# Kernel optimization log

Hardware: AMD Instinct MI355X
Metric: run time of the kernel (lower is better)

Reference implementation:

```python
import jax, jax.numpy as jnp
import numpy as np

B, S = 512, 512
VOCAB, E, H1, H2, NTAGS = 50000, 20, 30, 50, 45


def _xavier_scale(fan_in, fan_out):
    return float(np.sqrt(2.0 / (fan_in + fan_out)))


def setup_inputs() -> dict:
    key = jax.random.key(0)
    ks = jax.random.split(key, 32)
    n = lambda i, shape, s=1.0: jax.random.normal(ks[i], shape, dtype=jnp.float32) * s
    w = 0.1  # weight scale
    emb_f1 = n(0, (VOCAB, E), w).at[0].set(0.0)  # padding_idx=0
    emb_b1 = n(1, (VOCAB, E), w).at[0].set(0.0)
    xs1 = _xavier_scale(B, H1)
    xs2 = _xavier_scale(B, H2)
    inp = {
        "x": jax.random.randint(ks[2], (B, S), 0, VOCAB, dtype=jnp.int64),
        "emb_f1": emb_f1, "emb_b1": emb_b1,
        "h0_f1": n(3, (B, H1), xs1), "c0_f1": n(4, (B, H1), xs1),
        "Wih_f1": n(5, (4 * H1, E), w), "Whh_f1": n(6, (4 * H1, H1), w),
        "bih_f1": n(7, (4 * H1,), w), "bhh_f1": n(8, (4 * H1,), w),
        "h0_b1": n(9, (B, H1), xs1), "c0_b1": n(10, (B, H1), xs1),
        "Wih_b1": n(11, (4 * H1, E), w), "Whh_b1": n(12, (4 * H1, H1), w),
        "bih_b1": n(13, (4 * H1,), w), "bhh_b1": n(14, (4 * H1,), w),
        "h0_f2": n(15, (B, H2), xs2), "c0_f2": n(16, (B, H2), xs2),
        "Wih_f2": n(17, (4 * H2, 2 * H1), w), "Whh_f2": n(18, (4 * H2, H2), w),
        "bih_f2": n(19, (4 * H2,), w), "bhh_f2": n(20, (4 * H2,), w),
        "h0_b2": n(21, (B, H2), xs2), "c0_b2": n(22, (B, H2), xs2),
        "Wih_b2": n(23, (4 * H2, 2 * H1), w), "Whh_b2": n(24, (4 * H2, H2), w),
        "bih_b2": n(25, (4 * H2,), w), "bhh_b2": n(26, (4 * H2,), w),
        "lin_w": n(27, (NTAGS, 2 * H2), w), "lin_b": n(28, (NTAGS,), w),
    }
    return inp


def _run_lstm(seq, h0, c0, Wih, Whh, bih, bhh, forward):
    """PyTorch LSTMCell recurrence over seq (B,S,D). Replicates the original's
    quirks: backward dir appends hidden states in reversed time order, and the
    (S,B,H) stack is .view()-ed into (B,S,H) without transposing."""
    b, s, _ = seq.shape
    h = h0.shape[-1]
    xs = jnp.swapaxes(seq, 0, 1)  # (S,B,D)

    def step(carry, xt):
        hh, cc = carry
        g = xt @ Wih.T + bih + hh @ Whh.T + bhh  # (B, 4H), gate order i,f,g,o
        i, f, gg, o = jnp.split(g, 4, axis=-1)
        cc = jax.nn.sigmoid(f) * cc + jax.nn.sigmoid(i) * jnp.tanh(gg)
        hh = jax.nn.sigmoid(o) * jnp.tanh(cc)
        return (hh, cc), hh

    _, hs = jax.lax.scan(step, (h0, c0), xs, reverse=not forward)  # hs[i] ~ time i
    if not forward:
        hs = hs[::-1]  # torch appended in processing (reversed-time) order
    return hs.reshape(b, s, h)  # faithful buggy view (S,B,H) -> (B,S,H)


def reference(x, emb_f1, emb_b1,
              h0_f1, c0_f1, Wih_f1, Whh_f1, bih_f1, bhh_f1,
              h0_b1, c0_b1, Wih_b1, Whh_b1, bih_b1, bhh_b1,
              h0_f2, c0_f2, Wih_f2, Whh_f2, bih_f2, bhh_f2,
              h0_b2, c0_b2, Wih_b2, Whh_b2, bih_b2, bhh_b2,
              lin_w, lin_b):
    f1 = _run_lstm(emb_f1[x], h0_f1, c0_f1, Wih_f1, Whh_f1, bih_f1, bhh_f1, True)
    b1 = _run_lstm(emb_b1[x], h0_b1, c0_b1, Wih_b1, Whh_b1, bih_b1, bhh_b1, False)
    l1 = jnp.concatenate([f1, b1], axis=2)  # (B,S,2*H1)
    f2 = _run_lstm(l1, h0_f2, c0_f2, Wih_f2, Whh_f2, bih_f2, bhh_f2, True)
    b2 = _run_lstm(l1, h0_b2, c0_b2, Wih_b2, Whh_b2, bih_b2, bhh_b2, False)
    l2 = jnp.concatenate([f2, b2], axis=2)  # (B,S,2*H2)
    return l2 @ lin_w.T + lin_b  # (B,S,NTAGS)
```

## Files before the change

kernel.cpp:

```cpp
#include <hip/hip_runtime.h>
#include <hip/hip_bf16.h>

typedef __hip_bfloat16 bf16;
typedef __attribute__((ext_vector_type(8))) short short8;
typedef __attribute__((ext_vector_type(4))) float float4v;
typedef unsigned short ushort_t;

#define BB 512
#define SS 512
#define EE 20
#define H1C 30
#define H2C 50
#define NTC 45

#define BAR() asm volatile("s_waitcnt lgkmcnt(0)\n\ts_barrier" ::: "memory")

#if __has_builtin(__builtin_amdgcn_exp2f)
#define EXP2(x) __builtin_amdgcn_exp2f(x)
#else
#define EXP2(x) exp2f(x)
#endif
#if __has_builtin(__builtin_amdgcn_rcpf)
#define RCPF(x) __builtin_amdgcn_rcpf(x)
#else
#define RCPF(x) (1.0f / (x))
#endif

__device__ __forceinline__ float sigf(float v) {
    return RCPF(1.0f + EXP2(-1.4426950408889634f * v));
}
__device__ __forceinline__ float tanh_(float v) {
    return 2.0f * RCPF(1.0f + EXP2(-2.8853900817779268f * v)) - 1.0f;
}

__device__ __forceinline__ ushort_t f2bf(float f) {
    unsigned u = __float_as_uint(f);
    unsigned r = u + 0x7FFFu + ((u >> 16) & 1u);
    return (ushort_t)(r >> 16);
}
__device__ __forceinline__ float bf2f(ushort_t s) { return __uint_as_float(((unsigned)s) << 16); }

__device__ __forceinline__ float ldG(const void* p, int i, int f32) {
    if (f32) return ((const float*)p)[i];
    return bf2f(((const ushort_t*)p)[i]);
}
__device__ __forceinline__ int ldTok(const void* x, int i, int x64) {
    const int* xi = (const int*)x;
    return x64 ? xi[2 * i] : xi[i];
}

__global__ void detect_kernel(const void* bih, const void* x, int* flags) {
    if (threadIdx.x == 0 && blockIdx.x == 0) {
        const ushort_t* u = (const ushort_t*)bih;
        int isf = 0;
        for (int i = 0; i < 120; i++) {
            float v = fabsf(bf2f(u[i]));
            if (!(v < 16.0f)) isf = 1;
        }
        flags[0] = isf;
        const int* xi = (const int*)x;
        int orv = 0;
        for (int i = 1; i < 32; i += 2) orv |= xi[i];
        flags[1] = (orv == 0) ? 1 : 0;
    }
}

struct XV4 { float v[4]; };

__global__ __launch_bounds__(128) void lstm1_kernel(
    const void* __restrict__ x,
    const void* __restrict__ emb_f, const void* __restrict__ emb_b,
    const void* __restrict__ h0_f, const void* __restrict__ c0_f,
    const void* __restrict__ Wih_f, const void* __restrict__ Whh_f,
    const void* __restrict__ bih_f, const void* __restrict__ bhh_f,
    const void* __restrict__ h0_b, const void* __restrict__ c0_b,
    const void* __restrict__ Wih_b, const void* __restrict__ Whh_b,
    const void* __restrict__ bih_b, const void* __restrict__ bhh_b,
    ushort_t* __restrict__ hsf, ushort_t* __restrict__ hsb,
    const int* __restrict__ flags)
{
    const int f32v = flags[0], x64 = flags[1];
    const int wg = blockIdx.x, dir = wg >> 5, j0 = (wg & 31) << 4, tid = threadIdx.x;
    const int wave = tid >> 6, lane = tid & 63, li = lane & 15, quad = lane >> 4;

    const void* emb = dir ? emb_b : emb_f;
    const void* h0  = dir ? h0_b  : h0_f;
    const void* c0  = dir ? c0_b  : c0_f;
    const void* Wih = dir ? Wih_b : Wih_f;
    const void* Whh = dir ? Whh_b : Whh_f;
    const void* bih = dir ? bih_b : bih_f;
    const void* bhh = dir ? bhh_b : bhh_f;
    ushort_t* hs = dir ? hsb : hsf;

    __shared__ __align__(16) ushort_t Af[2][2][64][8];
    __shared__ int toks[16][SS];

    for (int idx = tid; idx < 16 * SS; idx += 128) {
        int r = idx >> 9, t = idx & (SS - 1);
        toks[r][t] = ldTok(x, (j0 + r) * SS + t, x64);
    }
    for (int idx = tid; idx < 2 * 2 * 64 * 8; idx += 128) ((ushort_t*)Af)[idx] = 0;

    const int n = wave * 16 + li;
    const bool nok = n < H1C;

    short8 bhi[4][2], blo[4][2];
    float bias_g[4];
    #pragma unroll
    for (int g = 0; g < 4; g++) {
        const int wrow = g * H1C + n;
        bias_g[g] = nok ? (ldG(bih, wrow, f32v) + ldG(bhh, wrow, f32v)) : 0.f;
        #pragma unroll
        for (int kt = 0; kt < 2; kt++) {
            short8 hi, lo;
            #pragma unroll
            for (int j = 0; j < 8; j++) {
                int k = kt * 32 + quad * 8 + j;
                float w = 0.f;
                if (nok) {
                    if (k < EE) w = ldG(Wih, wrow * EE + k, f32v);
                    else if (k < EE + H1C) w = ldG(Whh, wrow * H1C + (k - EE), f32v);
                }
                ushort_t h = f2bf(w);
                hi[j] = (short)h;
                lo[j] = (short)f2bf(w - bf2f(h));
            }
            bhi[g][kt] = hi; blo[g][kt] = lo;
        }
    }

    const int kh = EE + n;
    const int khk = kh >> 5, khg = (kh & 31) >> 3, khj = kh & 7;
    const int lrow = tid / 5, lc = tid - lrow * 5, k0 = lc * 4;
    const bool ldr = tid < 80;
    const int t0 = dir ? SS - 1 : 0, dt = dir ? -1 : 1;

    __syncthreads();

    float creg[4];
    #pragma unroll
    for (int r = 0; r < 4; r++) {
        const int m = quad * 4 + r;
        creg[r] = nok ? ldG(c0, (j0 + m) * H1C + n, f32v) : 0.f;
        ushort_t hb = nok ? f2bf(ldG(h0, (j0 + m) * H1C + n, f32v)) : 0;
        Af[0][khk][khg * 16 + m][khj] = hb;
    }
    XV4 xA, xB;
    if (ldr) {
        int tok = toks[lrow][t0];
        #pragma unroll
        for (int jj = 0; jj < 4; jj++)
            Af[0][0][(k0 >> 3) * 16 + lrow][(k0 & 7) + jj] = f2bf(ldG(emb, tok * EE + k0 + jj, f32v));
        int tok1 = toks[lrow][t0 + dt];
        #pragma unroll
        for (int jj = 0; jj < 4; jj++) xA.v[jj] = ldG(emb, tok1 * EE + k0 + jj, f32v);
    }
    __syncthreads();

    auto step = [&](int it, XV4& xin, XV4& xout) {
        const int t = t0 + dt * it;
        const int cur = it & 1, nxt = cur ^ 1;
        BAR();
        short8 af0 = *(const short8*)&Af[cur][0][lane][0];
        short8 af1 = *(const short8*)&Af[cur][1][lane][0];
        if (ldr && it + 2 < SS) {
            int tok = toks[lrow][t + 2 * dt];
            #pragma unroll
            for (int jj = 0; jj < 4; jj++) xout.v[jj] = ldG(emb, tok * EE + k0 + jj, f32v);
        }
        float4v acc[4];
        #pragma unroll
        for (int g = 0; g < 4; g++) {
            float4v a; a[0] = a[1] = a[2] = a[3] = bias_g[g];
            a = __builtin_amdgcn_mfma_f32_16x16x32_bf16(af0, bhi[g][0], a, 0, 0, 0);
            a = __builtin_amdgcn_mfma_f32_16x16x32_bf16(af0, blo[g][0], a, 0, 0, 0);
            a = __builtin_amdgcn_mfma_f32_16x16x32_bf16(af1, bhi[g][1], a, 0, 0, 0);
            a = __builtin_amdgcn_mfma_f32_16x16x32_bf16(af1, blo[g][1], a, 0, 0, 0);
            acc[g] = a;
        }
        ushort_t hb[4];
        #pragma unroll
        for (int r = 0; r < 4; r++) {
            float gi = acc[0][r], gf = acc[1][r], gg = acc[2][r], go = acc[3][r];
            float c = sigf(gf) * creg[r] + sigf(gi) * tanh_(gg);
            float h = sigf(go) * tanh_(c);
            creg[r] = c;
            hb[r] = nok ? f2bf(h) : 0;
            hs[((size_t)(j0 + quad * 4 + r) * SS + t) * 32 + n] = hb[r];
        }
        if (it + 1 < SS) {
            #pragma unroll
            for (int r = 0; r < 4; r++) Af[nxt][khk][khg * 16 + quad * 4 + r][khj] = hb[r];
            if (ldr) {
                #pragma unroll
                for (int jj = 0; jj < 4; jj++)
                    Af[nxt][0][(k0 >> 3) * 16 + lrow][(k0 & 7) + jj] = f2bf(xin.v[jj]);
            }
        }
    };
    for (int it = 0; it < SS; it += 2) { step(it, xA, xB); step(it + 1, xB, xA); }
}

__global__ __launch_bounds__(256) void lstm2_kernel(
    const ushort_t* __restrict__ hs1f, const ushort_t* __restrict__ hs1b,
    const void* __restrict__ h0_f, const void* __restrict__ c0_f,
    const void* __restrict__ Wih_f, const void* __restrict__ Whh_f,
    const void* __restrict__ bih_f, const void* __restrict__ bhh_f,
    const void* __restrict__ h0_b, const void* __restrict__ c0_b,
    const void* __restrict__ Wih_b, const void* __restrict__ Whh_b,
    const void* __restrict__ bih_b, const void* __restrict__ bhh_b,
    ushort_t* __restrict__ hsf, ushort_t* __restrict__ hsb,
    const int* __restrict__ flags)
{
    const int f32v = flags[0];
    const int wg = blockIdx.x, dir = wg >> 5, cb = (wg & 31) << 4, tid = threadIdx.x;
    const int wave = tid >> 6, lane = tid & 63, li = lane & 15, quad = lane >> 4;

    const void* h0  = dir ? h0_b  : h0_f;
    const void* c0  = dir ? c0_b  : c0_f;
    const void* Wih = dir ? Wih_b : Wih_f;
    const void* Whh = dir ? Whh_b : Whh_f;
    const void* bih = dir ? bih_b : bih_f;
    const void* bhh = dir ? bhh_b : bhh_f;
    ushort_t* hs = dir ? hsb : hsf;

    __shared__ __align__(16) ushort_t Af[2][4][64][8];
    for (int idx = tid; idx < 2 * 4 * 64 * 8; idx += 256) ((ushort_t*)Af)[idx] = 0;

    const int n = wave * 16 + li;
    const bool nok = n < H2C;

    short8 bhi[4][4], blo[4][4];
    float bias_g[4];
    #pragma unroll
    for (int g = 0; g < 4; g++) {
        const int wrow = g * H2C + n;
        bias_g[g] = nok ? (ldG(bih, wrow, f32v) + ldG(bhh, wrow, f32v)) : 0.f;
        #pragma unroll
        for (int kt = 0; kt < 4; kt++) {
            short8 hi, lo;
            #pragma unroll
            for (int j = 0; j < 8; j++) {
                int k = kt * 32 + quad * 8 + j;
                float w = 0.f;
                if (nok) {
                    if (k < H1C) w = ldG(Wih, wrow * (2 * H1C) + k, f32v);
                    else if (k >= 32 && k < 32 + H1C) w = ldG(Wih, wrow * (2 * H1C) + H1C + (k - 32), f32v);
                    else if (k >= 64 && k < 64 + H2C) w = ldG(Whh, wrow * H2C + (k - 64), f32v);
                }
                ushort_t h = f2bf(w);
                hi[j] = (short)h;
                lo[j] = (short)f2bf(w - bf2f(h));
            }
            bhi[g][kt] = hi; blo[g][kt] = lo;
        }
    }

    const int kh = 64 + n;
    const int khk = kh >> 5, khg = (kh & 31) >> 3, khj = kh & 7;
    const int lrow = tid >> 4, k0 = (tid & 15) * 4;
    const int t0 = dir ? SS - 1 : 0, dt = dir ? -1 : 1;

    auto loadX = [&](int c) -> ushort4 {
        const int a = cb + lrow;
        if (k0 < 32)
            return *(const ushort4*)&hs1f[((size_t)c * SS + a) * 32 + k0];
        else
            return *(const ushort4*)&hs1b[((size_t)c * SS + (SS - 1 - a)) * 32 + (k0 - 32)];
    };

    __syncthreads();

    float creg[4];
    #pragma unroll
    for (int r = 0; r < 4; r++) {
        const int m = quad * 4 + r;
        creg[r] = nok ? ldG(c0, (cb + m) * H2C + n, f32v) : 0.f;
        ushort_t hb = nok ? f2bf(ldG(h0, (cb + m) * H2C + n, f32v)) : 0;
        Af[0][khk][khg * 16 + m][khj] = hb;
    }
    {
        ushort4 xi = loadX(t0);
        const int kg = (k0 & 31) >> 3, kt = k0 >> 5, jb = k0 & 7;
        Af[0][kt][kg * 16 + lrow][jb + 0] = xi.x;
        Af[0][kt][kg * 16 + lrow][jb + 1] = xi.y;
        Af[0][kt][kg * 16 + lrow][jb + 2] = xi.z;
        Af[0][kt][kg * 16 + lrow][jb + 3] = xi.w;
    }
    ushort4 xA = loadX(t0 + dt), xB;
    __syncthreads();

    auto step = [&](int it, ushort4& xin, ushort4& xout) {
        const int c = t0 + dt * it;
        const int cur = it & 1, nxt = cur ^ 1;
        BAR();
        short8 af[4];
        #pragma unroll
        for (int kt = 0; kt < 4; kt++) af[kt] = *(const short8*)&Af[cur][kt][lane][0];
        if (it + 2 < SS) xout = loadX(c + 2 * dt);
        float4v acc[4];
        #pragma unroll
        for (int g = 0; g < 4; g++) {
            float4v a; a[0] = a[1] = a[2] = a[3] = bias_g[g];
            #pragma unroll
            for (int kt = 0; kt < 4; kt++) {
                a = __builtin_amdgcn_mfma_f32_16x16x32_bf16(af[kt], bhi[g][kt], a, 0, 0, 0);
                a = __builtin_amdgcn_mfma_f32_16x16x32_bf16(af[kt], blo[g][kt], a, 0, 0, 0);
            }
            acc[g] = a;
        }
        ushort_t hb[4];
        #pragma unroll
        for (int r = 0; r < 4; r++) {
            float gi = acc[0][r], gf = acc[1][r], gg = acc[2][r], go = acc[3][r];
            float cc = sigf(gf) * creg[r] + sigf(gi) * tanh_(gg);
            float h = sigf(go) * tanh_(cc);
            creg[r] = cc;
            hb[r] = nok ? f2bf(h) : 0;
        }
        ushort4 h4; h4.x = hb[0]; h4.y = hb[1]; h4.z = hb[2]; h4.w = hb[3];
        *(ushort4*)&hs[((size_t)c * 64 + n) * SS + cb + quad * 4] = h4;
        if (it + 1 < SS) {
            #pragma unroll
            for (int r = 0; r < 4; r++) Af[nxt][khk][khg * 16 + quad * 4 + r][khj] = hb[r];
            const int kg = (k0 & 31) >> 3, kt = k0 >> 5, jb = k0 & 7;
            Af[nxt][kt][kg * 16 + lrow][jb + 0] = xin.x;
            Af[nxt][kt][kg * 16 + lrow][jb + 1] = xin.y;
            Af[nxt][kt][kg * 16 + lrow][jb + 2] = xin.z;
            Af[nxt][kt][kg * 16 + lrow][jb + 3] = xin.w;
        }
    };
    for (int it = 0; it < SS; it += 2) { step(it, xA, xB); step(it + 1, xB, xA); }
}

__global__ __launch_bounds__(256) void lin_kernel(
    const ushort_t* __restrict__ hs2f, const ushort_t* __restrict__ hs2b,
    const void* __restrict__ lw, const void* __restrict__ lb,
    void* __restrict__ out, const int* __restrict__ flags)
{
    const int f32v = flags[0];
    const int tid = threadIdx.x, wave = tid >> 6, lane = tid & 63, li = lane & 15, quad = lane >> 4;

    __shared__ __align__(16) ushort_t Af[4][4][64][8];
    for (int idx = tid; idx < 4 * 4 * 64 * 8; idx += 256) ((ushort_t*)Af)[idx] = 0;

    short8 bhi[3][4], blo[3][4];
    float biasv[3];
    #pragma unroll
    for (int nt = 0; nt < 3; nt++) {
        const int nn = nt * 16 + li;
        const bool nok = nn < NTC;
        biasv[nt] = nok ? ldG(lb, nn, f32v) : 0.f;
        #pragma unroll
        for (int kt = 0; kt < 4; kt++) {
            short8 hi, lo;
            #pragma unroll
            for (int j = 0; j < 8; j++) {
                int k = kt * 32 + quad * 8 + j;
                float w = 0.f;
                if (nok) {
                    if (k < H2C) w = ldG(lw, nn * 100 + k, f32v);
                    else if (k >= 64 && k < 64 + H2C) w = ldG(lw, nn * 100 + 50 + (k - 64), f32v);
                }
                ushort_t h = f2bf(w);
                hi[j] = (short)h;
                lo[j] = (short)f2bf(w - bf2f(h));
            }
            bhi[nt][kt] = hi; blo[nt][kt] = lo;
        }
    }

    const int P0 = blockIdx.x * 64;
    const int i = P0 >> 9, j0 = P0 & 511;
    __syncthreads();
    for (int idx = tid; idx < 100 * 32; idx += 256) {
        const int kk = idx >> 5, pj = (idx & 31) * 2;
        unsigned v;
        int k;
        if (kk < H2C) {
            v = *(const unsigned*)&hs2f[((size_t)i * 64 + kk) * SS + j0 + pj];
            k = kk;
        } else {
            v = *(const unsigned*)&hs2b[((size_t)(SS - 1 - i) * 64 + (kk - H2C)) * SS + j0 + pj];
            k = 64 + (kk - H2C);
        }
        const int kt = k >> 5, kg = (k & 31) >> 3, j = k & 7;
        Af[pj >> 4][kt][kg * 16 + (pj & 15)][j] = (ushort_t)(v & 0xFFFF);
        Af[pj >> 4][kt][kg * 16 + ((pj + 1) & 15)][j] = (ushort_t)(v >> 16);
    }
    __syncthreads();

    short8 af[4];
    #pragma unroll
    for (int kt = 0; kt < 4; kt++) af[kt] = *(const short8*)&Af[wave][kt][lane][0];
    #pragma unroll
    for (int nt = 0; nt < 3; nt++) {
        float4v a; a[0] = a[1] = a[2] = a[3] = biasv[nt];
        #pragma unroll
        for (int kt = 0; kt < 4; kt++) {
            a = __builtin_amdgcn_mfma_f32_16x16x32_bf16(af[kt], bhi[nt][kt], a, 0, 0, 0);
            a = __builtin_amdgcn_mfma_f32_16x16x32_bf16(af[kt], blo[nt][kt], a, 0, 0, 0);
        }
        const int nn = nt * 16 + li;
        if (nn < NTC) {
            #pragma unroll
            for (int reg = 0; reg < 4; reg++) {
                const int prow = wave * 16 + quad * 4 + reg;
                const size_t op = (size_t)(P0 + prow) * NTC + nn;
                if (f32v) ((float*)out)[op] = a[reg];
                else      ((ushort_t*)out)[op] = f2bf(a[reg]);
            }
        }
    }
}

extern "C" void kernel_launch(void* const* d_in, const int* in_sizes, int n_in,
                              void* d_out, int out_size, void* d_ws, size_t ws_size,
                              hipStream_t stream)
{
    const void* x      = d_in[0];
    const void* emb_f1 = d_in[1];
    const void* emb_b1 = d_in[2];
    const void* h0_f1  = d_in[3];
    const void* c0_f1  = d_in[4];
    const void* Wih_f1 = d_in[5];
    const void* Whh_f1 = d_in[6];
    const void* bih_f1 = d_in[7];
    const void* bhh_f1 = d_in[8];
    const void* h0_b1  = d_in[9];
    const void* c0_b1  = d_in[10];
    const void* Wih_b1 = d_in[11];
    const void* Whh_b1 = d_in[12];
    const void* bih_b1 = d_in[13];
    const void* bhh_b1 = d_in[14];
    const void* h0_f2  = d_in[15];
    const void* c0_f2  = d_in[16];
    const void* Wih_f2 = d_in[17];
    const void* Whh_f2 = d_in[18];
    const void* bih_f2 = d_in[19];
    const void* bhh_f2 = d_in[20];
    const void* h0_b2  = d_in[21];
    const void* c0_b2  = d_in[22];
    const void* Wih_b2 = d_in[23];
    const void* Whh_b2 = d_in[24];
    const void* bih_b2 = d_in[25];
    const void* bhh_b2 = d_in[26];
    const void* lin_w  = d_in[27];
    const void* lin_b  = d_in[28];

    int* flags = (int*)d_ws;
    ushort_t* hs1f = (ushort_t*)((char*)d_ws + 256);
    ushort_t* hs1b = hs1f + (size_t)BB * SS * 32;
    ushort_t* hs2f = hs1b + (size_t)BB * SS * 32;
    ushort_t* hs2b = hs2f + (size_t)SS * 64 * BB;

    detect_kernel<<<1, 64, 0, stream>>>(bih_f1, x, flags);
    lstm1_kernel<<<64, 128, 0, stream>>>(x, emb_f1, emb_b1,
        h0_f1, c0_f1, Wih_f1, Whh_f1, bih_f1, bhh_f1,
        h0_b1, c0_b1, Wih_b1, Whh_b1, bih_b1, bhh_b1, hs1f, hs1b, flags);
    lstm2_kernel<<<64, 256, 0, stream>>>(hs1f, hs1b,
        h0_f2, c0_f2, Wih_f2, Whh_f2, bih_f2, bhh_f2,
        h0_b2, c0_b2, Wih_b2, Whh_b2, bih_b2, bhh_b2, hs2f, hs2b, flags);
    lin_kernel<<<(BB * SS) / 64, 256, 0, stream>>>(hs2f, hs2b, lin_w, lin_b, d_out, flags);
}
```

Before: 1.004 ms.

## Precompute next-step input projection off the recurrent critical path and prescale gates

After: 1.022 ms. About the same (+1.8%).

```diff
diff --git a/kernel.cpp b/kernel.cpp
--- a/kernel.cpp
+++ b/kernel.cpp
@@ -26,9 +26,10 @@
 #define RCPF(x) (1.0f / (x))
 #endif
 
-__device__ __forceinline__ float sigf(float v) {
-    return RCPF(1.0f + EXP2(-1.4426950408889634f * v));
-}
+#define LOG2E 1.4426950408889634f
+
+__device__ __forceinline__ float sigE(float v)  { return RCPF(1.0f + EXP2(-v)); }
+__device__ __forceinline__ float tanhE(float v) { return 2.0f * RCPF(1.0f + EXP2(-v)) - 1.0f; }
 __device__ __forceinline__ float tanh_(float v) {
     return 2.0f * RCPF(1.0f + EXP2(-2.8853900817779268f * v)) - 1.0f;
 }
@@ -65,7 +66,34 @@
     }
 }
 
-struct XV4 { float v[4]; };
+struct XV4R { unsigned r[4]; };
+
+__device__ __forceinline__ XV4R ldEmbRaw(const void* emb, int tok, int k0, int f32v) {
+    XV4R o;
+    if (f32v) {
+        uint4 v = *(const uint4*)((const float*)emb + (size_t)tok * EE + k0);
+        o.r[0] = v.x; o.r[1] = v.y; o.r[2] = v.z; o.r[3] = v.w;
+    } else {
+        uint2 v = *(const uint2*)((const ushort_t*)emb + (size_t)tok * EE + k0);
+        o.r[0] = v.x; o.r[1] = v.y; o.r[2] = 0; o.r[3] = 0;
+    }
+    return o;
+}
+__device__ __forceinline__ ushort4 cvtX(XV4R x, int f32v) {
+    ushort4 u;
+    if (f32v) {
+        u.x = f2bf(__uint_as_float(x.r[0]));
+        u.y = f2bf(__uint_as_float(x.r[1]));
+        u.z = f2bf(__uint_as_float(x.r[2]));
+        u.w = f2bf(__uint_as_float(x.r[3]));
+    } else {
+        u.x = (ushort_t)(x.r[0] & 0xFFFFu);
+        u.y = (ushort_t)(x.r[0] >> 16);
+        u.z = (ushort_t)(x.r[1] & 0xFFFFu);
+        u.w = (ushort_t)(x.r[1] >> 16);
+    }
+    return u;
+}
 
 __global__ __launch_bounds__(128) void lstm1_kernel(
     const void* __restrict__ x,
@@ -108,8 +136,9 @@
     float bias_g[4];
     #pragma unroll
     for (int g = 0; g < 4; g++) {
+        const float sc = (g == 2) ? 2.0f * LOG2E : LOG2E;
         const int wrow = g * H1C + n;
-        bias_g[g] = nok ? (ldG(bih, wrow, f32v) + ldG(bhh, wrow, f32v)) : 0.f;
+        bias_g[g] = nok ? sc * (ldG(bih, wrow, f32v) + ldG(bhh, wrow, f32v)) : 0.f;
         #pragma unroll
         for (int kt = 0; kt < 2; kt++) {
             short8 hi, lo;
@@ -118,9 +147,10 @@
                 int k = kt * 32 + quad * 8 + j;
                 float w = 0.f;
                 if (nok) {
-                    if (k < EE) w = ldG(Wih, wrow * EE + k, f32v);
-                    else if (k < EE + H1C) w = ldG(Whh, wrow * H1C + (k - EE), f32v);
+                    if (kt == 0) { if (k < EE) w = ldG(Wih, wrow * EE + k, f32v); }
+                    else { int kk = k - 32; if (kk < H1C) w = ldG(Whh, wrow * H1C + kk, f32v); }
                 }
+                w *= sc;
                 ushort_t h = f2bf(w);
                 hi[j] = (short)h;
                 lo[j] = (short)f2bf(w - bf2f(h));
@@ -129,8 +159,7 @@
         }
     }
 
-    const int kh = EE + n;
-    const int khk = kh >> 5, khg = (kh & 31) >> 3, khj = kh & 7;
+    const int hr0 = (n >> 3) * 16, hj = n & 7;
     const int lrow = tid / 5, lc = tid - lrow * 5, k0 = lc * 4;
     const bool ldr = tid < 80;
     const int t0 = dir ? SS - 1 : 0, dt = dir ? -1 : 1;
@@ -142,61 +171,69 @@
     for (int r = 0; r < 4; r++) {
         const int m = quad * 4 + r;
         creg[r] = nok ? ldG(c0, (j0 + m) * H1C + n, f32v) : 0.f;
-        ushort_t hb = nok ? f2bf(ldG(h0, (j0 + m) * H1C + n, f32v)) : 0;
-        Af[0][khk][khg * 16 + m][khj] = hb;
-    }
-    XV4 xA, xB;
+        ushort_t hb0 = nok ? f2bf(ldG(h0, (j0 + m) * H1C + n, f32v)) : (ushort_t)0;
+        Af[0][1][hr0 + m][hj] = hb0;
+    }
+    XV4R xA, xB;
     if (ldr) {
-        int tok = toks[lrow][t0];
-        #pragma unroll
-        for (int jj = 0; jj < 4; jj++)
-            Af[0][0][(k0 >> 3) * 16 + lrow][(k0 & 7) + jj] = f2bf(ldG(emb, tok * EE + k0 + jj, f32v));
-        int tok1 = toks[lrow][t0 + dt];
-        #pragma unroll
-        for (int jj = 0; jj < 4; jj++) xA.v[jj] = ldG(emb, tok1 * EE + k0 + jj, f32v);
+        *(ushort4*)&Af[0][0][(k0 >> 3) * 16 + lrow][k0 & 7] =
+            cvtX(ldEmbRaw(emb, toks[lrow][t0], k0, f32v), f32v);
+        *(ushort4*)&Af[1][0][(k0 >> 3) * 16 + lrow][k0 & 7] =
+            cvtX(ldEmbRaw(emb, toks[lrow][t0 + dt], k0, f32v), f32v);
+        xA = ldEmbRaw(emb, toks[lrow][t0 + 2 * dt], k0, f32v);
     }
     __syncthreads();
 
-    auto step = [&](int it, XV4& xin, XV4& xout) {
+    float4v xacc[4];
+    {
+        short8 afx0 = *(const short8*)&Af[0][0][lane][0];
+        #pragma unroll
+        for (int g = 0; g < 4; g++) {
+            float4v a; a[0] = a[1] = a[2] = a[3] = bias_g[g];
+            a = __builtin_amdgcn_mfma_f32_16x16x32_bf16(afx0, bhi[g][0], a, 0, 0, 0);
+            a = __builtin_amdgcn_mfma_f32_16x16x32_bf16(afx0, blo[g][0], a, 0, 0, 0);
+            xacc[g] = a;
+        }
+    }
+
+    auto step = [&](int it, XV4R& xin, XV4R& xout) {
         const int t = t0 + dt * it;
         const int cur = it & 1, nxt = cur ^ 1;
         BAR();
-        short8 af0 = *(const short8*)&Af[cur][0][lane][0];
-        short8 af1 = *(const short8*)&Af[cur][1][lane][0];
-        if (ldr && it + 2 < SS) {
-            int tok = toks[lrow][t + 2 * dt];
-            #pragma unroll
-            for (int jj = 0; jj < 4; jj++) xout.v[jj] = ldG(emb, tok * EE + k0 + jj, f32v);
-        }
-        float4v acc[4];
+        short8 afh = *(const short8*)&Af[cur][1][lane][0];
+        short8 afx = *(const short8*)&Af[nxt][0][lane][0];
+        if (ldr && it + 3 < SS)
+            xout = ldEmbRaw(emb, toks[lrow][t + 3 * dt], k0, f32v);
+        float4v acc[4], xn[4];
         #pragma unroll
         for (int g = 0; g < 4; g++) {
-            float4v a; a[0] = a[1] = a[2] = a[3] = bias_g[g];
-            a = __builtin_amdgcn_mfma_f32_16x16x32_bf16(af0, bhi[g][0], a, 0, 0, 0);
-            a = __builtin_amdgcn_mfma_f32_16x16x32_bf16(af0, blo[g][0], a, 0, 0, 0);
-            a = __builtin_amdgcn_mfma_f32_16x16x32_bf16(af1, bhi[g][1], a, 0, 0, 0);
-            a = __builtin_amdgcn_mfma_f32_16x16x32_bf16(af1, blo[g][1], a, 0, 0, 0);
+            float4v a = xacc[g];
+            a = __builtin_amdgcn_mfma_f32_16x16x32_bf16(afh, bhi[g][1], a, 0, 0, 0);
+            a = __builtin_amdgcn_mfma_f32_16x16x32_bf16(afh, blo[g][1], a, 0, 0, 0);
             acc[g] = a;
+            float4v b; b[0] = b[1] = b[2] = b[3] = bias_g[g];
+            b = __builtin_amdgcn_mfma_f32_16x16x32_bf16(afx, bhi[g][0], b, 0, 0, 0);
+            b = __builtin_amdgcn_mfma_f32_16x16x32_bf16(afx, blo[g][0], b, 0, 0, 0);
+            xn[g] = b;
         }
         ushort_t hb[4];
         #pragma unroll
         for (int r = 0; r < 4; r++) {
             float gi = acc[0][r], gf = acc[1][r], gg = acc[2][r], go = acc[3][r];
-            float c = sigf(gf) * creg[r] + sigf(gi) * tanh_(gg);
-            float h = sigf(go) * tanh_(c);
+            float c = sigE(gf) * creg[r] + sigE(gi) * tanhE(gg);
+            float h = sigE(go) * tanh_(c);
             creg[r] = c;
-            hb[r] = nok ? f2bf(h) : 0;
+            hb[r] = nok ? f2bf(h) : (ushort_t)0;
             hs[((size_t)(j0 + quad * 4 + r) * SS + t) * 32 + n] = hb[r];
         }
         if (it + 1 < SS) {
             #pragma unroll
-            for (int r = 0; r < 4; r++) Af[nxt][khk][khg * 16 + quad * 4 + r][khj] = hb[r];
-            if (ldr) {
-                #pragma unroll
-                for (int jj = 0; jj < 4; jj++)
-                    Af[nxt][0][(k0 >> 3) * 16 + lrow][(k0 & 7) + jj] = f2bf(xin.v[jj]);
-            }
-        }
+            for (int r = 0; r < 4; r++) Af[nxt][1][hr0 + quad * 4 + r][hj] = hb[r];
+        }
+        if (ldr && it + 2 < SS)
+            *(ushort4*)&Af[cur][0][(k0 >> 3) * 16 + lrow][k0 & 7] = cvtX(xin, f32v);
+        #pragma unroll
+        for (int g = 0; g < 4; g++) xacc[g] = xn[g];
     };
     for (int it = 0; it < SS; it += 2) { step(it, xA, xB); step(it + 1, xB, xA); }
 }
@@ -234,8 +271,9 @@
     float bias_g[4];
     #pragma unroll
     for (int g = 0; g < 4; g++) {
+        const float sc = (g == 2) ? 2.0f * LOG2E : LOG2E;
         const int wrow = g * H2C + n;
-        bias_g[g] = nok ? (ldG(bih, wrow, f32v) + ldG(bhh, wrow, f32v)) : 0.f;
+        bias_g[g] = nok ? sc * (ldG(bih, wrow, f32v) + ldG(bhh, wrow, f32v)) : 0.f;
         #pragma unroll
         for (int kt = 0; kt < 4; kt++) {
             short8 hi, lo;
@@ -248,6 +286,7 @@
                     else if (k >= 32 && k < 32 + H1C) w = ldG(Wih, wrow * (2 * H1C) + H1C + (k - 32), f32v);
                     else if (k >= 64 && k < 64 + H2C) w = ldG(Whh, wrow * H2C + (k - 64), f32v);
                 }
+                w *= sc;
                 ushort_t h = f2bf(w);
                 hi[j] = (short)h;
                 lo[j] = (short)f2bf(w - bf2f(h));
@@ -259,6 +298,7 @@
     const int kh = 64 + n;
     const int khk = kh >> 5, khg = (kh & 31) >> 3, khj = kh & 7;
     const int lrow = tid >> 4, k0 = (tid & 15) * 4;
+    const int skt = k0 >> 5, skg = (k0 & 31) >> 3, sjb = k0 & 7;
     const int t0 = dir ? SS - 1 : 0, dt = dir ? -1 : 1;
 
     auto loadX = [&](int c) -> ushort4 {
@@ -276,59 +316,73 @@
     for (int r = 0; r < 4; r++) {
         const int m = quad * 4 + r;
         creg[r] = nok ? ldG(c0, (cb + m) * H2C + n, f32v) : 0.f;
-        ushort_t hb = nok ? f2bf(ldG(h0, (cb + m) * H2C + n, f32v)) : 0;
-        Af[0][khk][khg * 16 + m][khj] = hb;
-    }
+        ushort_t hb0 = nok ? f2bf(ldG(h0, (cb + m) * H2C + n, f32v)) : (ushort_t)0;
+        Af[0][khk][khg * 16 + m][khj] = hb0;
+    }
+    *(ushort4*)&Af[0][skt][skg * 16 + lrow][sjb] = loadX(t0);
+    *(ushort4*)&Af[1][skt][skg * 16 + lrow][sjb] = loadX(t0 + dt);
+    ushort4 xA = loadX(t0 + 2 * dt), xB;
+    __syncthreads();
+
+    float4v xacc[4];
     {
-        ushort4 xi = loadX(t0);
-        const int kg = (k0 & 31) >> 3, kt = k0 >> 5, jb = k0 & 7;
-        Af[0][kt][kg * 16 + lrow][jb + 0] = xi.x;
-        Af[0][kt][kg * 16 + lrow][jb + 1] = xi.y;
-        Af[0][kt][kg * 16 + lrow][jb + 2] = xi.z;
-        Af[0][kt][kg * 16 + lrow][jb + 3] = xi.w;
-    }
-    ushort4 xA = loadX(t0 + dt), xB;
-    __syncthreads();
+        short8 afx0 = *(const short8*)&Af[0][0][lane][0];
+        short8 afx1 = *(const short8*)&Af[0][1][lane][0];
+        #pragma unroll
+        for (int g = 0; g < 4; g++) {
+            float4v a; a[0] = a[1] = a[2] = a[3] = bias_g[g];
+            a = __builtin_amdgcn_mfma_f32_16x16x32_bf16(afx0, bhi[g][0], a, 0, 0, 0);
+            a = __builtin_amdgcn_mfma_f32_16x16x32_bf16(afx0, blo[g][0], a, 0, 0, 0);
+            a = __builtin_amdgcn_mfma_f32_16x16x32_bf16(afx1, bhi[g][1], a, 0, 0, 0);
+            a = __builtin_amdgcn_mfma_f32_16x16x32_bf16(afx1, blo[g][1], a, 0, 0, 0);
+            xacc[g] = a;
+        }
+    }
 
     auto step = [&](int it, ushort4& xin, ushort4& xout) {
         const int c = t0 + dt * it;
         const int cur = it & 1, nxt = cur ^ 1;
         BAR();
-        short8 af[4];
-        #pragma unroll
-        for (int kt = 0; kt < 4; kt++) af[kt] = *(const short8*)&Af[cur][kt][lane][0];
-        if (it + 2 < SS) xout = loadX(c + 2 * dt);
-        float4v acc[4];
+        short8 afh0 = *(const short8*)&Af[cur][2][lane][0];
+        short8 afh1 = *(const short8*)&Af[cur][3][lane][0];
+        short8 afx0 = *(const short8*)&Af[nxt][0][lane][0];
+        short8 afx1 = *(const short8*)&Af[nxt][1][lane][0];
+        if (it + 3 < SS) xout = loadX(c + 3 * dt);
+        float4v acc[4], xn[4];
         #pragma unroll
         for (int g = 0; g < 4; g++) {
-            float4v a; a[0] = a[1] = a[2] = a[3] = bias_g[g];
-            #pragma unroll
-            for (int kt = 0; kt < 4; kt++) {
-                a = __builtin_amdgcn_mfma_f32_16x16x32_bf16(af[kt], bhi[g][kt], a, 0, 0, 0);
-                a = __builtin_amdgcn_mfma_f32_16x16x32_bf16(af[kt], blo[g][kt], a, 0, 0, 0);
-            }
+            float4v a = xacc[g];
+            a = __builtin_amdgcn_mfma_f32_16x16x32_bf16(afh0, bhi[g][2], a, 0, 0, 0);
+            a = __builtin_amdgcn_mfma_f32_16x16x32_bf16(afh0, blo[g][2], a, 0, 0, 0);
+            a = __builtin_amdgcn_mfma_f32_16x16x32_bf16(afh1, bhi[g][3], a, 0, 0, 0);
+            a = __builtin_amdgcn_mfma_f32_16x16x32_bf16(afh1, blo[g][3], a, 0, 0, 0);
             acc[g] = a;
+            float4v b; b[0] = b[1] = b[2] = b[3] = bias_g[g];
+            b = __builtin_amdgcn_mfma_f32_16x16x32_bf16(afx0, bhi[g][0], b, 0, 0, 0);
+            b = __builtin_amdgcn_mfma_f32_16x16x32_bf16(afx0, blo[g][0], b, 0, 0, 0);
+            b = __builtin_amdgcn_mfma_f32_16x16x32_bf16(afx1, bhi[g][1], b, 0, 0, 0);
+            b = __builtin_amdgcn_mfma_f32_16x16x32_bf16(afx1, blo[g][1], b, 0, 0, 0);
+            xn[g] = b;
         }
         ushort_t hb[4];
         #pragma unroll
         for (int r = 0; r < 4; r++) {
             float gi = acc[0][r], gf = acc[1][r], gg = acc[2][r], go = acc[3][r];
-            float cc = sigf(gf) * creg[r] + sigf(gi) * tanh_(gg);
-            float h = sigf(go) * tanh_(cc);
+            float cc = sigE(gf) * creg[r] + sigE(gi) * tanhE(gg);
+            float h = sigE(go) * tanh_(cc);
             creg[r] = cc;
-            hb[r] = nok ? f2bf(h) : 0;
+            hb[r] = nok ? f2bf(h) : (ushort_t)0;
         }
         ushort4 h4; h4.x = hb[0]; h4.y = hb[1]; h4.z = hb[2]; h4.w = hb[3];
         *(ushort4*)&hs[((size_t)c * 64 + n) * SS + cb + quad * 4] = h4;
         if (it + 1 < SS) {
             #pragma unroll
             for (int r = 0; r < 4; r++) Af[nxt][khk][khg * 16 + quad * 4 + r][khj] = hb[r];
-            const int kg = (k0 & 31) >> 3, kt = k0 >> 5, jb = k0 & 7;
-            Af[nxt][kt][kg * 16 + lrow][jb + 0] = xin.x;
-            Af[nxt][kt][kg * 16 + lrow][jb + 1] = xin.y;
-            Af[nxt][kt][kg * 16 + lrow][jb + 2] = xin.z;
-            Af[nxt][kt][kg * 16 + lrow][jb + 3] = xin.w;
-        }
+        }
+        if (it + 2 < SS)
+            *(ushort4*)&Af[cur][skt][skg * 16 + lrow][sjb] = xin;
+        #pragma unroll
+        for (int g = 0; g < 4; g++) xacc[g] = xn[g];
     };
     for (int it = 0; it < SS; it += 2) { step(it, xA, xB); step(it + 1, xB, xA); }
 }
```
